# Kernel optimization log

Measured on AMD Instinct MI355X. Metric: run time of the kernel, lower is better.

The kernel has to match this reference:

```python
import jax, jax.numpy as jnp
import numpy as np

T, B, I, H, L = 512, 4096, 23, 20, 2  # seq len, batch, input dim, hidden dim, num layers


def setup_inputs() -> dict:
    key = jax.random.key(0)
    ks = jax.random.split(key, 13)
    s = 1.0 / np.sqrt(H)  # pytorch default uniform bound scale (use normal*s for simplicity)
    f32 = jnp.float32
    return {
        "x": jax.random.normal(ks[0], (T, B, I), f32),
        "h0": jax.random.normal(ks[1], (L, B, H), f32),
        "c0": jax.random.normal(ks[2], (L, B, H), f32),
        "W_ih0": jax.random.normal(ks[3], (4 * H, I), f32) * s,
        "W_hh0": jax.random.normal(ks[4], (4 * H, H), f32) * s,
        "b_ih0": jax.random.normal(ks[5], (4 * H,), f32) * s,
        "b_hh0": jax.random.normal(ks[6], (4 * H,), f32) * s,
        "W_ih1": jax.random.normal(ks[7], (4 * H, H), f32) * s,
        "W_hh1": jax.random.normal(ks[8], (4 * H, H), f32) * s,
        "b_ih1": jax.random.normal(ks[9], (4 * H,), f32) * s,
        "b_hh1": jax.random.normal(ks[10], (4 * H,), f32) * s,
        "W_lin": jax.random.normal(ks[11], (1, H), f32) * s,
        "b_lin": jax.random.normal(ks[12], (1,), f32) * s,
    }


def _lstm_layer(xs, h0, c0, W_ih, W_hh, b_ih, b_hh):
    # Precompute input contributions for all timesteps at once: [T, B, 4H]
    xg = jnp.einsum('tbi,gi->tbg', xs, W_ih) + b_ih + b_hh

    def step(carry, xg_t):
        h, c = carry
        gates = xg_t + h @ W_hh.T          # [B, 4H]
        i, f, g, o = jnp.split(gates, 4, axis=-1)  # pytorch gate order: i, f, g, o
        c = jax.nn.sigmoid(f) * c + jax.nn.sigmoid(i) * jnp.tanh(g)
        h = jax.nn.sigmoid(o) * jnp.tanh(c)
        return (h, c), h

    _, hs = jax.lax.scan(step, (h0, c0), xg)
    return hs  # [T, B, H]


def reference(x, h0, c0, W_ih0, W_hh0, b_ih0, b_hh0, W_ih1, W_hh1, b_ih1, b_hh1, W_lin, b_lin):
    out = _lstm_layer(x, h0[0], c0[0], W_ih0, W_hh0, b_ih0, b_hh0)
    out = _lstm_layer(out, h0[1], c0[1], W_ih1, W_hh1, b_ih1, b_hh1)
    y = jax.nn.relu(out)                   # relu(lstm output), [T, B, H]
    # lin applied then time-index 6 selected; equivalent (and cheaper) to index first
    z6 = y[6] @ W_lin.T + b_lin            # [B, 1]
    return jax.nn.relu(z6)
```

## Files before the change

kernel.cpp:

```cpp
#include <hip/hip_runtime.h>
#include <math.h>


constexpr int kT  = 7;
constexpr int kI  = 23;
constexpr int kH  = 20;
constexpr int kG  = 80;
constexpr int kBT = 8;
constexpr int kThreads = 320;
constexpr int kXP = 24;
constexpr int kGP = 10;

__device__ __forceinline__ float sigm(float v) {
    return __builtin_amdgcn_rcpf(1.0f + __builtin_amdgcn_exp2f(v * -1.44269504f));
}
__device__ __forceinline__ float tanh_(float v) {
    return 1.0f - 2.0f * __builtin_amdgcn_rcpf(__builtin_amdgcn_exp2f(v * 2.88539008f) + 1.0f);
}
template<int J>
__device__ __forceinline__ float qb(float v) {
    return __int_as_float(__builtin_amdgcn_mov_dpp(__float_as_int(v), J * 0x55, 0xF, 0xF, true));
}
__device__ __forceinline__ float rotl(float v) {
    return __int_as_float(__builtin_amdgcn_mov_dpp(__float_as_int(v), 0x39, 0xF, 0xF, true));
}
__device__ __forceinline__ float4 rot4(float4 v) {
    return make_float4(rotl(v.x), rotl(v.y), rotl(v.z), rotl(v.w));
}
__device__ __forceinline__ void lstm_update(float a, float& c, float& h) {
    const float gi = qb<0>(a), gf = qb<1>(a), gg = qb<2>(a), go = qb<3>(a);
    c = sigm(gf) * c + sigm(gi) * tanh_(gg);
    h = sigm(go) * tanh_(c);
}

__device__ __forceinline__ float dot20(const float* __restrict__ row, const float* w, int q4) {
    float4 v = *reinterpret_cast<const float4*>(row + q4);
    float a0 = 0.f, a1 = 0.f;
    a0 = fmaf(w[0],  v.x, a0); a1 = fmaf(w[1],  v.y, a1);
    a0 = fmaf(w[2],  v.z, a0); a1 = fmaf(w[3],  v.w, a1);
    v = rot4(v);
    a0 = fmaf(w[4],  v.x, a0); a1 = fmaf(w[5],  v.y, a1);
    a0 = fmaf(w[6],  v.z, a0); a1 = fmaf(w[7],  v.w, a1);
    v = rot4(v);
    a0 = fmaf(w[8],  v.x, a0); a1 = fmaf(w[9],  v.y, a1);
    a0 = fmaf(w[10], v.z, a0); a1 = fmaf(w[11], v.w, a1);
    v = rot4(v);
    a0 = fmaf(w[12], v.x, a0); a1 = fmaf(w[13], v.y, a1);
    a0 = fmaf(w[14], v.z, a0); a1 = fmaf(w[15], v.w, a1);
    const float4 t = *reinterpret_cast<const float4*>(row + 16);
    a0 = fmaf(w[16], t.x, a0); a1 = fmaf(w[17], t.y, a1);
    a0 = fmaf(w[18], t.z, a0); a1 = fmaf(w[19], t.w, a1);
    return a0 + a1;
}

__device__ __forceinline__ float dot24(const float* __restrict__ row, const float* w, int q4) {
    float4 v = *reinterpret_cast<const float4*>(row + q4);
    float a0 = 0.f, a1 = 0.f;
    a0 = fmaf(w[0],  v.x, a0); a1 = fmaf(w[1],  v.y, a1);
    a0 = fmaf(w[2],  v.z, a0); a1 = fmaf(w[3],  v.w, a1);
    v = rot4(v);
    a0 = fmaf(w[4],  v.x, a0); a1 = fmaf(w[5],  v.y, a1);
    a0 = fmaf(w[6],  v.z, a0); a1 = fmaf(w[7],  v.w, a1);
    v = rot4(v);
    a0 = fmaf(w[8],  v.x, a0); a1 = fmaf(w[9],  v.y, a1);
    a0 = fmaf(w[10], v.z, a0); a1 = fmaf(w[11], v.w, a1);
    v = rot4(v);
    a0 = fmaf(w[12], v.x, a0); a1 = fmaf(w[13], v.y, a1);
    a0 = fmaf(w[14], v.z, a0); a1 = fmaf(w[15], v.w, a1);
    const float4 t4 = *reinterpret_cast<const float4*>(row + 16);
    a0 = fmaf(w[16], t4.x, a0); a1 = fmaf(w[17], t4.y, a1);
    a0 = fmaf(w[18], t4.z, a0); a1 = fmaf(w[19], t4.w, a1);
    const float4 t5 = *reinterpret_cast<const float4*>(row + 20);
    a0 = fmaf(w[20], t5.x, a0); a1 = fmaf(w[21], t5.y, a1);
    a0 = fmaf(w[22], t5.z, a0); a1 = fmaf(w[23], t5.w, a1);
    return a0 + a1;
}

__global__ __launch_bounds__(kThreads, 2) void lstm7_kernel(
    const float* __restrict__ x,
    const float* __restrict__ h0,
    const float* __restrict__ c0,
    const float* __restrict__ Wih0,
    const float* __restrict__ Whh0,
    const float* __restrict__ bih0,
    const float* __restrict__ bhh0,
    const float* __restrict__ Wih1,
    const float* __restrict__ Whh1,
    const float* __restrict__ bih1,
    const float* __restrict__ bhh1,
    const float* __restrict__ Wlin,
    const float* __restrict__ blin,
    float* __restrict__ out,
    int B)
{
    __shared__ __align__(16) float xS[kT][kBT][kXP];
    __shared__ __align__(16) float xgS[kT][kG][kGP];
    __shared__ __align__(16) float h1S[2][kBT][kH];
    __shared__ __align__(16) float h2S[2][kBT][kH];

    const int tid = threadIdx.x;
    const int b0  = blockIdx.x * kBT;
    const int bp  = tid / kG;
    const int q   = tid & 3;
    const int u   = (tid % kG) >> 2;
    const int grow = q * kH + u;
    const int bb  = bp * 2;
    const int q4  = q * 4;

    for (int idx = tid; idx < kT * kBT * kI; idx += kThreads) {
        const int t = idx / (kBT * kI);
        const int r = idx % (kBT * kI);
        const int b = r / kI;
        const int i = r % kI;
        xS[t][b][i] = x[((size_t)t * B + b0 + b) * kI + i];
    }
    if (tid < kT * kBT) xS[tid / kBT][tid % kBT][kI] = 0.0f;

    if (tid < kH * kBT) {
        const int b = tid / kH, uu = tid % kH;
        h1S[0][b][uu] = h0[(size_t)(b0 + b) * kH + uu];
        h2S[0][b][uu] = h0[(size_t)(B + b0 + b) * kH + uu];
    }

    __syncthreads();

    {
        float wA[24];
        const float* WA = Wih0 + grow * kI;
#pragma unroll
        for (int r = 0; r < 4; ++r) {
            const int c = (q + r) & 3;
            wA[4*r+0] = WA[4*c+0]; wA[4*r+1] = WA[4*c+1];
            wA[4*r+2] = WA[4*c+2]; wA[4*r+3] = WA[4*c+3];
        }
        wA[16] = WA[16]; wA[17] = WA[17]; wA[18] = WA[18]; wA[19] = WA[19];
        wA[20] = WA[20]; wA[21] = WA[21]; wA[22] = WA[22]; wA[23] = 0.0f;
        const float bias1 = bih0[grow] + bhh0[grow];
#pragma unroll
        for (int t = 0; t < kT; ++t) {
            const float g0 = bias1 + dot24(&xS[t][bb][0],     wA, q4);
            const float g1 = bias1 + dot24(&xS[t][bb + 1][0], wA, q4);
            *reinterpret_cast<float2*>(&xgS[t][grow][bb]) = make_float2(g0, g1);
        }
    }

    float wB[kH], wC[kH], wD[kH];
    {
        const float4* PB = reinterpret_cast<const float4*>(Whh0 + grow * kH);
        const float4* PC = reinterpret_cast<const float4*>(Wih1 + grow * kH);
        const float4* PD = reinterpret_cast<const float4*>(Whh1 + grow * kH);
#pragma unroll
        for (int r = 0; r < 4; ++r) {
            const int c = (q + r) & 3;
            const float4 vb = PB[c], vc = PC[c], vd = PD[c];
            wB[4*r+0]=vb.x; wB[4*r+1]=vb.y; wB[4*r+2]=vb.z; wB[4*r+3]=vb.w;
            wC[4*r+0]=vc.x; wC[4*r+1]=vc.y; wC[4*r+2]=vc.z; wC[4*r+3]=vc.w;
            wD[4*r+0]=vd.x; wD[4*r+1]=vd.y; wD[4*r+2]=vd.z; wD[4*r+3]=vd.w;
        }
        const float4 tb = PB[4], tc = PC[4], td = PD[4];
        wB[16]=tb.x; wB[17]=tb.y; wB[18]=tb.z; wB[19]=tb.w;
        wC[16]=tc.x; wC[17]=tc.y; wC[18]=tc.z; wC[19]=tc.w;
        wD[16]=td.x; wD[17]=td.y; wD[18]=td.z; wD[19]=td.w;
    }
    const float bias2 = bih1[grow] + bhh1[grow];
    float c1x = c0[(size_t)(b0 + bb) * kH + u];
    float c1y = c0[(size_t)(b0 + bb + 1) * kH + u];
    float c2x = c0[(size_t)(B + b0 + bb) * kH + u];
    float c2y = c0[(size_t)(B + b0 + bb + 1) * kH + u];

#pragma unroll
    for (int t = 0; t < kT; ++t) {
        const int rb = t & 1, wb = rb ^ 1;

        const float2 xg = *reinterpret_cast<const float2*>(&xgS[t][grow][bb]);
        const float g0 = xg.x + dot20(&h1S[rb][bb][0],     wB, q4);
        const float g1 = xg.y + dot20(&h1S[rb][bb + 1][0], wB, q4);
        float h1x, h1y;
        lstm_update(g0, c1x, h1x);
        lstm_update(g1, c1y, h1y);
        if (q == 0) { h1S[wb][bb][u] = h1x; h1S[wb][bb + 1][u] = h1y; }
        __syncthreads();

        const float s0 = bias2 + dot20(&h1S[wb][bb][0],     wC, q4)
                               + dot20(&h2S[rb][bb][0],     wD, q4);
        const float s1 = bias2 + dot20(&h1S[wb][bb + 1][0], wC, q4)
                               + dot20(&h2S[rb][bb + 1][0], wD, q4);
        float h2x, h2y;
        lstm_update(s0, c2x, h2x);
        lstm_update(s1, c2y, h2y);
        if (q == 0) { h2S[wb][bb][u] = h2x; h2S[wb][bb + 1][u] = h2y; }
        __syncthreads();
    }

    if (tid < kBT) {
        const int b = tid;
        float acc = blin[0];
#pragma unroll
        for (int uu = 0; uu < kH; ++uu) {
            acc = fmaf(fmaxf(h2S[1][b][uu], 0.0f), Wlin[uu], acc);
        }
        out[b0 + b] = fmaxf(acc, 0.0f);
    }
}

extern "C" void kernel_launch(void* const* d_in, const int* in_sizes, int n_in,
                              void* d_out, int out_size, void* d_ws, size_t ws_size,
                              hipStream_t stream) {
    const float* x    = (const float*)d_in[0];
    const float* h0   = (const float*)d_in[1];
    const float* c0   = (const float*)d_in[2];
    const float* Wih0 = (const float*)d_in[3];
    const float* Whh0 = (const float*)d_in[4];
    const float* bih0 = (const float*)d_in[5];
    const float* bhh0 = (const float*)d_in[6];
    const float* Wih1 = (const float*)d_in[7];
    const float* Whh1 = (const float*)d_in[8];
    const float* bih1 = (const float*)d_in[9];
    const float* bhh1 = (const float*)d_in[10];
    const float* Wlin = (const float*)d_in[11];
    const float* blin = (const float*)d_in[12];
    float* out = (float*)d_out;

    const int B = in_sizes[1] / (2 * kH);
    const int blocks = B / kBT;

    hipLaunchKernelGGL(lstm7_kernel, dim3(blocks), dim3(kThreads), 0, stream,
                       x, h0, c0, Wih0, Whh0, bih0, bhh0,
                       Wih1, Whh1, bih1, bhh1, Wlin, blin, out, B);
}
```

Before: 28.66 us.

## Prepack LSTM weights in a separate kernel and read x directly from global

Adds a single-block pack kernel that rearranges all LSTM weight matrices and summed biases into a coalesced float4 workspace layout, pre-rotated for the DPP dot product. The main kernel loads its weights with coalesced float4 reads instead of strided per-row loads. It also drops the shared-memory staging of x and the barrier that followed it, computing the layer-0 input projection straight from global memory. The trade-offs are an extra kernel launch on the stream and uncoalesced per-thread scalar reads of x.

```diff
diff --git a/kernel.cpp b/kernel.cpp
--- a/kernel.cpp
+++ b/kernel.cpp
@@ -8,8 +8,10 @@
 constexpr int kG  = 80;
 constexpr int kBT = 8;
 constexpr int kThreads = 320;
-constexpr int kXP = 24;
 constexpr int kGP = 10;
+constexpr int kSlots = 21;
+constexpr int kB1Off = kSlots * kG * 4;
+constexpr int kB2Off = kB1Off + kG;
 
 __device__ __forceinline__ float sigm(float v) {
     return __builtin_amdgcn_rcpf(1.0f + __builtin_amdgcn_exp2f(v * -1.44269504f));
@@ -53,126 +55,120 @@
     return a0 + a1;
 }
 
-__device__ __forceinline__ float dot24(const float* __restrict__ row, const float* w, int q4) {
-    float4 v = *reinterpret_cast<const float4*>(row + q4);
-    float a0 = 0.f, a1 = 0.f;
-    a0 = fmaf(w[0],  v.x, a0); a1 = fmaf(w[1],  v.y, a1);
-    a0 = fmaf(w[2],  v.z, a0); a1 = fmaf(w[3],  v.w, a1);
-    v = rot4(v);
-    a0 = fmaf(w[4],  v.x, a0); a1 = fmaf(w[5],  v.y, a1);
-    a0 = fmaf(w[6],  v.z, a0); a1 = fmaf(w[7],  v.w, a1);
-    v = rot4(v);
-    a0 = fmaf(w[8],  v.x, a0); a1 = fmaf(w[9],  v.y, a1);
-    a0 = fmaf(w[10], v.z, a0); a1 = fmaf(w[11], v.w, a1);
-    v = rot4(v);
-    a0 = fmaf(w[12], v.x, a0); a1 = fmaf(w[13], v.y, a1);
-    a0 = fmaf(w[14], v.z, a0); a1 = fmaf(w[15], v.w, a1);
-    const float4 t4 = *reinterpret_cast<const float4*>(row + 16);
-    a0 = fmaf(w[16], t4.x, a0); a1 = fmaf(w[17], t4.y, a1);
-    a0 = fmaf(w[18], t4.z, a0); a1 = fmaf(w[19], t4.w, a1);
-    const float4 t5 = *reinterpret_cast<const float4*>(row + 20);
-    a0 = fmaf(w[20], t5.x, a0); a1 = fmaf(w[21], t5.y, a1);
-    a0 = fmaf(w[22], t5.z, a0); a1 = fmaf(w[23], t5.w, a1);
-    return a0 + a1;
+__global__ void pack_kernel(const float* __restrict__ Wih0,
+                            const float* __restrict__ Whh0,
+                            const float* __restrict__ bih0,
+                            const float* __restrict__ bhh0,
+                            const float* __restrict__ Wih1,
+                            const float* __restrict__ Whh1,
+                            const float* __restrict__ bih1,
+                            const float* __restrict__ bhh1,
+                            float* __restrict__ ws)
+{
+    const int tid = threadIdx.x;
+    for (int idx = tid; idx < kSlots * kG; idx += 256) {
+        const int slot = idx / kG, p = idx % kG;
+        const int q = p & 3, u = p >> 2, g = q * kH + u;
+        float4 v;
+        if (slot < 6) {
+            const float* W = Wih0 + g * kI;
+            const int c = slot * 4;
+            v.x = W[c];
+            v.y = (c + 1 < kI) ? W[c + 1] : 0.0f;
+            v.z = (c + 2 < kI) ? W[c + 2] : 0.0f;
+            v.w = (c + 3 < kI) ? W[c + 3] : 0.0f;
+        } else {
+            const int m = (slot - 6) / 5, r = (slot - 6) % 5;
+            const float* W = (m == 0 ? Whh0 : (m == 1 ? Wih1 : Whh1)) + g * kH;
+            const int c = (r < 4) ? 4 * ((q + r) & 3) : 16;
+            v = make_float4(W[c], W[c + 1], W[c + 2], W[c + 3]);
+        }
+        reinterpret_cast<float4*>(ws)[idx] = v;
+    }
+    if (tid < 2 * kG) {
+        const int p = tid % kG, g = (p & 3) * kH + (p >> 2);
+        ws[kB1Off + tid] = (tid < kG) ? (bih0[g] + bhh0[g]) : (bih1[g] + bhh1[g]);
+    }
 }
 
 __global__ __launch_bounds__(kThreads, 2) void lstm7_kernel(
     const float* __restrict__ x,
     const float* __restrict__ h0,
     const float* __restrict__ c0,
-    const float* __restrict__ Wih0,
-    const float* __restrict__ Whh0,
-    const float* __restrict__ bih0,
-    const float* __restrict__ bhh0,
-    const float* __restrict__ Wih1,
-    const float* __restrict__ Whh1,
-    const float* __restrict__ bih1,
-    const float* __restrict__ bhh1,
     const float* __restrict__ Wlin,
     const float* __restrict__ blin,
+    const float* __restrict__ ws,
     float* __restrict__ out,
     int B)
 {
-    __shared__ __align__(16) float xS[kT][kBT][kXP];
     __shared__ __align__(16) float xgS[kT][kG][kGP];
     __shared__ __align__(16) float h1S[2][kBT][kH];
     __shared__ __align__(16) float h2S[2][kBT][kH];
 
     const int tid = threadIdx.x;
     const int b0  = blockIdx.x * kBT;
+    const int p   = tid % kG;
+    const int q   = p & 3;
+    const int u   = p >> 2;
     const int bp  = tid / kG;
-    const int q   = tid & 3;
-    const int u   = (tid % kG) >> 2;
-    const int grow = q * kH + u;
     const int bb  = bp * 2;
     const int q4  = q * 4;
 
-    for (int idx = tid; idx < kT * kBT * kI; idx += kThreads) {
-        const int t = idx / (kBT * kI);
-        const int r = idx % (kBT * kI);
-        const int b = r / kI;
-        const int i = r % kI;
-        xS[t][b][i] = x[((size_t)t * B + b0 + b) * kI + i];
-    }
-    if (tid < kT * kBT) xS[tid / kBT][tid % kBT][kI] = 0.0f;
-
-    if (tid < kH * kBT) {
-        const int b = tid / kH, uu = tid % kH;
-        h1S[0][b][uu] = h0[(size_t)(b0 + b) * kH + uu];
-        h2S[0][b][uu] = h0[(size_t)(B + b0 + b) * kH + uu];
-    }
-
-    __syncthreads();
+    if (tid < kBT * kH) {
+        const int e = tid / kH, uu = tid % kH;
+        h1S[0][e][uu] = h0[(size_t)(b0 + e) * kH + uu];
+        h2S[0][e][uu] = h0[((size_t)B + b0 + e) * kH + uu];
+    }
+
+    const float4* pk = reinterpret_cast<const float4*>(ws);
 
     {
         float wA[24];
-        const float* WA = Wih0 + grow * kI;
-#pragma unroll
-        for (int r = 0; r < 4; ++r) {
-            const int c = (q + r) & 3;
-            wA[4*r+0] = WA[4*c+0]; wA[4*r+1] = WA[4*c+1];
-            wA[4*r+2] = WA[4*c+2]; wA[4*r+3] = WA[4*c+3];
-        }
-        wA[16] = WA[16]; wA[17] = WA[17]; wA[18] = WA[18]; wA[19] = WA[19];
-        wA[20] = WA[20]; wA[21] = WA[21]; wA[22] = WA[22]; wA[23] = 0.0f;
-        const float bias1 = bih0[grow] + bhh0[grow];
+#pragma unroll
+        for (int j = 0; j < 6; ++j) {
+            const float4 v = pk[j * kG + p];
+            wA[4*j] = v.x; wA[4*j+1] = v.y; wA[4*j+2] = v.z; wA[4*j+3] = v.w;
+        }
+        const float bias1 = ws[kB1Off + p];
 #pragma unroll
         for (int t = 0; t < kT; ++t) {
-            const float g0 = bias1 + dot24(&xS[t][bb][0],     wA, q4);
-            const float g1 = bias1 + dot24(&xS[t][bb + 1][0], wA, q4);
-            *reinterpret_cast<float2*>(&xgS[t][grow][bb]) = make_float2(g0, g1);
+#pragma unroll
+            for (int e = 0; e < 2; ++e) {
+                const float* xr = x + ((size_t)t * B + b0 + bb + e) * kI;
+                float a0 = bias1, a1 = 0.f;
+#pragma unroll
+                for (int i = 0; i < kI; i += 2) {
+                    a0 = fmaf(wA[i], xr[i], a0);
+                    if (i + 1 < kI) a1 = fmaf(wA[i + 1], xr[i + 1], a1);
+                }
+                xgS[t][p][bb + e] = a0 + a1;
+            }
         }
     }
 
     float wB[kH], wC[kH], wD[kH];
-    {
-        const float4* PB = reinterpret_cast<const float4*>(Whh0 + grow * kH);
-        const float4* PC = reinterpret_cast<const float4*>(Wih1 + grow * kH);
-        const float4* PD = reinterpret_cast<const float4*>(Whh1 + grow * kH);
-#pragma unroll
-        for (int r = 0; r < 4; ++r) {
-            const int c = (q + r) & 3;
-            const float4 vb = PB[c], vc = PC[c], vd = PD[c];
-            wB[4*r+0]=vb.x; wB[4*r+1]=vb.y; wB[4*r+2]=vb.z; wB[4*r+3]=vb.w;
-            wC[4*r+0]=vc.x; wC[4*r+1]=vc.y; wC[4*r+2]=vc.z; wC[4*r+3]=vc.w;
-            wD[4*r+0]=vd.x; wD[4*r+1]=vd.y; wD[4*r+2]=vd.z; wD[4*r+3]=vd.w;
-        }
-        const float4 tb = PB[4], tc = PC[4], td = PD[4];
-        wB[16]=tb.x; wB[17]=tb.y; wB[18]=tb.z; wB[19]=tb.w;
-        wC[16]=tc.x; wC[17]=tc.y; wC[18]=tc.z; wC[19]=tc.w;
-        wD[16]=td.x; wD[17]=td.y; wD[18]=td.z; wD[19]=td.w;
-    }
-    const float bias2 = bih1[grow] + bhh1[grow];
+#pragma unroll
+    for (int j = 0; j < 5; ++j) {
+        const float4 vb = pk[(6 + j)  * kG + p];
+        const float4 vc = pk[(11 + j) * kG + p];
+        const float4 vd = pk[(16 + j) * kG + p];
+        wB[4*j]=vb.x; wB[4*j+1]=vb.y; wB[4*j+2]=vb.z; wB[4*j+3]=vb.w;
+        wC[4*j]=vc.x; wC[4*j+1]=vc.y; wC[4*j+2]=vc.z; wC[4*j+3]=vc.w;
+        wD[4*j]=vd.x; wD[4*j+1]=vd.y; wD[4*j+2]=vd.z; wD[4*j+3]=vd.w;
+    }
+    const float bias2 = ws[kB2Off + p];
     float c1x = c0[(size_t)(b0 + bb) * kH + u];
     float c1y = c0[(size_t)(b0 + bb + 1) * kH + u];
-    float c2x = c0[(size_t)(B + b0 + bb) * kH + u];
-    float c2y = c0[(size_t)(B + b0 + bb + 1) * kH + u];
+    float c2x = c0[((size_t)B + b0 + bb) * kH + u];
+    float c2y = c0[((size_t)B + b0 + bb + 1) * kH + u];
+
+    __syncthreads();
 
 #pragma unroll
     for (int t = 0; t < kT; ++t) {
         const int rb = t & 1, wb = rb ^ 1;
 
-        const float2 xg = *reinterpret_cast<const float2*>(&xgS[t][grow][bb]);
+        const float2 xg = *reinterpret_cast<const float2*>(&xgS[t][p][bb]);
         const float g0 = xg.x + dot20(&h1S[rb][bb][0],     wB, q4);
         const float g1 = xg.y + dot20(&h1S[rb][bb + 1][0], wB, q4);
         float h1x, h1y;
@@ -220,11 +216,13 @@
     const float* Wlin = (const float*)d_in[11];
     const float* blin = (const float*)d_in[12];
     float* out = (float*)d_out;
+    float* ws  = (float*)d_ws;
 
     const int B = in_sizes[1] / (2 * kH);
     const int blocks = B / kBT;
 
+    hipLaunchKernelGGL(pack_kernel, dim3(1), dim3(256), 0, stream,
+                       Wih0, Whh0, bih0, bhh0, Wih1, Whh1, bih1, bhh1, ws);
     hipLaunchKernelGGL(lstm7_kernel, dim3(blocks), dim3(kThreads), 0, stream,
-                       x, h0, c0, Wih0, Whh0, bih0, bhh0,
-                       Wih1, Whh1, bih1, bhh1, Wlin, blin, out, B);
-}
+                       x, h0, c0, Wlin, blin, ws, out, B);
+}
```

Result: slower. 39.44 us (+37.6%).
